# Kernel tuning notes

Measured on AMD Instinct MI355X. Metric: run time of the kernel, lower is better.

## Reference

```python
import jax, jax.numpy as jnp
import numpy as np

NUM_LAYERS = 3
CHANNELS = 8
IN_CHANNELS = 8
MASK_OUT_STRIDE = 4
WEIGHT_NUMS = [(IN_CHANNELS + 2) * CHANNELS, CHANNELS * CHANNELS, CHANNELS]
BIAS_NUMS = [CHANNELS, CHANNELS, 1]
NUM_GEN_PARAMS = sum(WEIGHT_NUMS) + sum(BIAS_NUMS)  # 169
SOI = np.array([64.0, 128.0, 256.0, 512.0, 1024.0], dtype=np.float32)


def compute_locations(h, w, stride):
    # FCOS grid point centers, (H*W, 2) in (x, y) order
    shifts_x = jnp.arange(w, dtype=jnp.float32) * stride + stride // 2
    shifts_y = jnp.arange(h, dtype=jnp.float32) * stride + stride // 2
    ys, xs = jnp.meshgrid(shifts_y, shifts_x, indexing='ij')
    return jnp.stack([xs.reshape(-1), ys.reshape(-1)], axis=1)


def parse_dynamic_params(params):
    # params: (n_inst, 169) -> per-layer weights (n, cout, cin) and biases (n, cout)
    n = params.shape[0]
    split_pts = np.cumsum(WEIGHT_NUMS + BIAS_NUMS)[:-1].tolist()
    splits = jnp.split(params, split_pts, axis=1)
    ws, bs = [], []
    for l in range(NUM_LAYERS):
        cout = CHANNELS if l < NUM_LAYERS - 1 else 1
        ws.append(splits[l].reshape(n, cout, -1))
        bs.append(splits[NUM_LAYERS + l].reshape(n, cout))
    return ws, bs


def aligned_bilinear(x, factor):
    # Faithful port of AdelaiDet aligned_bilinear (replicate pad + align_corners=True bilinear).
    if factor == 1:
        return x
    n, c, h, w = x.shape
    xp = jnp.pad(x, ((0, 0), (0, 0), (0, 1), (0, 1)), mode='edge')  # (n,c,h+1,w+1)
    oh, ow = factor * h + 1, factor * w + 1
    # align_corners=True with oh = factor*h+1 over h+1 samples -> exact coords i/factor
    ys = jnp.arange(oh, dtype=x.dtype) / factor
    xs = jnp.arange(ow, dtype=x.dtype) / factor
    y0 = jnp.floor(ys).astype(jnp.int32)
    y1 = jnp.minimum(y0 + 1, h)
    x0 = jnp.floor(xs).astype(jnp.int32)
    x1 = jnp.minimum(x0 + 1, w)
    wy = (ys - y0.astype(x.dtype))[None, None, :, None]
    wx = (xs - x0.astype(x.dtype))[None, None, None, :]
    rows = xp[:, :, y0, :] * (1 - wy) + xp[:, :, y1, :] * wy
    out = rows[:, :, :, x0] * (1 - wx) + rows[:, :, :, x1] * wx
    pad = factor // 2
    out = jnp.pad(out, ((0, 0), (0, 0), (pad, 0), (pad, 0)), mode='edge')
    return out[:, :, :oh - 1, :ow - 1]  # (n, c, factor*h, factor*w)


def dynamic_head(x, params):
    # x: (n_inst, cin, HW); per-instance 1x1 convs == batched tiny GEMMs
    ws, bs = parse_dynamic_params(params)
    h = x
    for i, (w, b) in enumerate(zip(ws, bs)):
        h = jnp.einsum('noi,nip->nop', w, h) + b[:, :, None]
        if i < NUM_LAYERS - 1:
            h = jax.nn.relu(h)
    return h  # (n_inst, 1, HW)


def setup_inputs() -> dict:
    key = jax.random.key(0)
    k = jax.random.split(key, 6)
    N, H, W, n_inst = 2, 200, 200, 128
    return {
        'mask_feats': jax.random.normal(k[0], (N, IN_CHANNELS, H, W), jnp.float32),
        'mask_head_params': jax.random.normal(k[1], (n_inst, NUM_GEN_PARAMS), jnp.float32) * 0.1,
        'boundary_head_params': jax.random.normal(k[2], (n_inst, NUM_GEN_PARAMS), jnp.float32) * 0.1,
        'instance_locations': jax.random.uniform(k[3], (n_inst, 2), jnp.float32) * 1600.0,
        'im_inds': jax.random.randint(k[4], (n_inst,), 0, N),
        'fpn_levels': jax.random.randint(k[5], (n_inst,), 0, 5),
        'mask_feat_stride': 8,
    }


def reference(mask_feats, mask_head_params, boundary_head_params, instance_locations, im_inds, fpn_levels, mask_feat_stride):
    N, C, H, W = mask_feats.shape
    n_inst = mask_head_params.shape[0]
    locs = compute_locations(H, W, mask_feat_stride)                 # (HW, 2)
    rel = instance_locations[:, None, :] - locs[None, :, :]          # (n, HW, 2)
    rel = jnp.transpose(rel, (0, 2, 1))                              # (n, 2, HW)
    soi = jnp.asarray(SOI)[fpn_levels]                               # (n,)
    rel = (rel / soi[:, None, None]).astype(mask_feats.dtype)
    feats = mask_feats[im_inds].reshape(n_inst, C, H * W)            # per-instance gather
    x = jnp.concatenate([rel, feats], axis=1)                        # (n, C+2, HW)
    factor = mask_feat_stride // MASK_OUT_STRIDE
    m = aligned_bilinear(dynamic_head(x, mask_head_params).reshape(n_inst, 1, H, W), factor)
    bd = aligned_bilinear(dynamic_head(x, boundary_head_params).reshape(n_inst, 1, H, W), factor)
    return jax.nn.sigmoid(m), jax.nn.sigmoid(bd)
```

## Files before the change

kernel.cpp:

```cpp
#include <hip/hip_runtime.h>


#define BLOCK 256
#define Hh 200
#define Ww 200
#define CINCH 8
#define NP 169
#define TH 25
#define MAXR 14
#define OW 400
#define OH 400

typedef float f32x4 __attribute__((ext_vector_type(4)));
typedef float f32x2 __attribute__((ext_vector_type(2)));

__device__ __forceinline__ f32x2 splat2(float v) { f32x2 r; r.x = v; r.y = v; return r; }
__device__ __forceinline__ f32x2 pkfma(f32x2 a, f32x2 b, f32x2 c) {
    return __builtin_elementwise_fma(a, b, c);
}

__global__ __launch_bounds__(BLOCK, 3) void dmh_fused(
    const float* __restrict__ mask_feats,
    const float* __restrict__ mparams,
    const float* __restrict__ bparams,
    const float* __restrict__ ilocs,
    const int*   __restrict__ im_inds,
    const int*   __restrict__ fpn_levels,
    const int*   __restrict__ stride_p,
    float* __restrict__ out,
    int n_inst)
{
    __shared__ __align__(16) float s_par[2 * 192];
    __shared__ __align__(16) float s_m[2][MAXR][Ww];

    const int tid  = threadIdx.x;
    const int tile = blockIdx.x;
    const int inst = blockIdx.y;

    for (int j = tid; j < 2 * NP; j += BLOCK) {
        const int head = (j < NP) ? 0 : 1;
        const int k = j - head * NP;
        const float v = head ? bparams[inst * NP + k] : mparams[inst * NP + k];
        int dst;
        if      (k < 80)  dst = (k / 10) * 12 + (k % 10);
        else if (k < 144) dst = 96 + (k - 80);
        else if (k < 152) dst = 160 + (k - 144);
        else if (k < 160) dst = 168 + (k - 152);
        else if (k < 168) dst = 176 + (k - 160);
        else              dst = 184;
        s_par[head * 192 + dst] = v;
    }

    const int   s    = stride_p[0];
    const int   half = s >> 1;
    const int   im   = im_inds[inst];
    const int   lvl  = fpn_levels[inst];
    const float inv_soi = 1.0f / (float)(64 << lvl);
    const float ixl = ilocs[inst * 2 + 0];
    const float iyl = ilocs[inst * 2 + 1];

    const int i0 = tile * TH;
    const int r_begin = ((i0 > 0) ? (i0 - 1) : 0) >> 1;
    int r_end = ((i0 + TH - 2) >> 1) + 1;
    if (r_end > Hh - 1) r_end = Hh - 1;
    const int nrows = r_end - r_begin + 1;

    __syncthreads();

    const int npx = nrows * Ww;
    const float* fbase = mask_feats + (size_t)im * CINCH * Hh * Ww;

    for (int g = tid * 4; g < npx; g += BLOCK * 4) {
        asm volatile("" ::: "memory");

        const int lr = g / Ww;
        const int c  = g - lr * Ww;
        const int r  = r_begin + lr;

        f32x2 xa[10], xb[10];
        {
            const float ry   = (iyl - (float)(r * s + half)) * inv_soi;
            const float step = -(float)s * inv_soi;
            const float cx0  = (ixl - (float)(c * s + half)) * inv_soi;
            xa[0].x = cx0;            xa[0].y = cx0 + step;
            xb[0].x = cx0 + 2*step;   xb[0].y = cx0 + 3*step;
            xa[1] = splat2(ry);       xb[1] = xa[1];
            const float* fp = fbase + r * Ww + c;
            #pragma unroll
            for (int ch = 0; ch < 8; ch++) {
                const f32x4 f = *(const f32x4*)(fp + ch * (Hh * Ww));
                xa[2 + ch].x = f.x; xa[2 + ch].y = f.y;
                xb[2 + ch].x = f.z; xb[2 + ch].y = f.w;
            }
        }

        #pragma unroll 1
        for (int head = 0; head < 2; head++) {
            const float* P = s_par + head * 192;
            const f32x2 zero = splat2(0.0f);

            f32x2 h1a[8], h1b[8];
            #pragma unroll
            for (int o = 0; o < 8; o++) {
                const f32x4 wa = *(const f32x4*)(P + o * 12);
                const f32x4 wb = *(const f32x4*)(P + o * 12 + 4);
                const float w8 = P[o * 12 + 8];
                const float w9 = P[o * 12 + 9];
                f32x2 aa = splat2(P[168 + o]);
                f32x2 ab = aa;
                aa = pkfma(splat2(wa.x), xa[0], aa); ab = pkfma(splat2(wa.x), xb[0], ab);
                aa = pkfma(splat2(wa.y), xa[1], aa); ab = pkfma(splat2(wa.y), xb[1], ab);
                aa = pkfma(splat2(wa.z), xa[2], aa); ab = pkfma(splat2(wa.z), xb[2], ab);
                aa = pkfma(splat2(wa.w), xa[3], aa); ab = pkfma(splat2(wa.w), xb[3], ab);
                aa = pkfma(splat2(wb.x), xa[4], aa); ab = pkfma(splat2(wb.x), xb[4], ab);
                aa = pkfma(splat2(wb.y), xa[5], aa); ab = pkfma(splat2(wb.y), xb[5], ab);
                aa = pkfma(splat2(wb.z), xa[6], aa); ab = pkfma(splat2(wb.z), xb[6], ab);
                aa = pkfma(splat2(wb.w), xa[7], aa); ab = pkfma(splat2(wb.w), xb[7], ab);
                aa = pkfma(splat2(w8),   xa[8], aa); ab = pkfma(splat2(w8),   xb[8], ab);
                aa = pkfma(splat2(w9),   xa[9], aa); ab = pkfma(splat2(w9),   xb[9], ab);
                h1a[o] = __builtin_elementwise_max(aa, zero);
                h1b[o] = __builtin_elementwise_max(ab, zero);
            }

            f32x2 h2a[8], h2b[8];
            #pragma unroll
            for (int o = 0; o < 8; o++) {
                const f32x4 wa = *(const f32x4*)(P + 96 + o * 8);
                const f32x4 wb = *(const f32x4*)(P + 96 + o * 8 + 4);
                f32x2 aa = splat2(P[176 + o]);
                f32x2 ab = aa;
                aa = pkfma(splat2(wa.x), h1a[0], aa); ab = pkfma(splat2(wa.x), h1b[0], ab);
                aa = pkfma(splat2(wa.y), h1a[1], aa); ab = pkfma(splat2(wa.y), h1b[1], ab);
                aa = pkfma(splat2(wa.z), h1a[2], aa); ab = pkfma(splat2(wa.z), h1b[2], ab);
                aa = pkfma(splat2(wa.w), h1a[3], aa); ab = pkfma(splat2(wa.w), h1b[3], ab);
                aa = pkfma(splat2(wb.x), h1a[4], aa); ab = pkfma(splat2(wb.x), h1b[4], ab);
                aa = pkfma(splat2(wb.y), h1a[5], aa); ab = pkfma(splat2(wb.y), h1b[5], ab);
                aa = pkfma(splat2(wb.z), h1a[6], aa); ab = pkfma(splat2(wb.z), h1b[6], ab);
                aa = pkfma(splat2(wb.w), h1a[7], aa); ab = pkfma(splat2(wb.w), h1b[7], ab);
                h2a[o] = __builtin_elementwise_max(aa, zero);
                h2b[o] = __builtin_elementwise_max(ab, zero);
            }

            const f32x4 wa = *(const f32x4*)(P + 160);
            const f32x4 wb = *(const f32x4*)(P + 164);
            f32x2 aa = splat2(P[184]);
            f32x2 ab = aa;
            aa = pkfma(splat2(wa.x), h2a[0], aa); ab = pkfma(splat2(wa.x), h2b[0], ab);
            aa = pkfma(splat2(wa.y), h2a[1], aa); ab = pkfma(splat2(wa.y), h2b[1], ab);
            aa = pkfma(splat2(wa.z), h2a[2], aa); ab = pkfma(splat2(wa.z), h2b[2], ab);
            aa = pkfma(splat2(wa.w), h2a[3], aa); ab = pkfma(splat2(wa.w), h2b[3], ab);
            aa = pkfma(splat2(wb.x), h2a[4], aa); ab = pkfma(splat2(wb.x), h2b[4], ab);
            aa = pkfma(splat2(wb.y), h2a[5], aa); ab = pkfma(splat2(wb.y), h2b[5], ab);
            aa = pkfma(splat2(wb.z), h2a[6], aa); ab = pkfma(splat2(wb.z), h2b[6], ab);
            aa = pkfma(splat2(wb.w), h2a[7], aa); ab = pkfma(splat2(wb.w), h2b[7], ab);

            f32x4 res;
            res.x = aa.x; res.y = aa.y; res.z = ab.x; res.w = ab.y;
            *(f32x4*)(&s_m[head][lr][c]) = res;
        }
    }

    __syncthreads();

    float* out0 = out + (size_t)inst * (OH * OW) + (size_t)i0 * OW;
    float* out1 = out0 + (size_t)n_inst * (OH * OW);

    const int NU = OW / 8;
    const int ntask = TH * NU;
    for (int t = tid; t < ntask; t += BLOCK) {
        const int row = t / NU;
        const int u   = t - row * NU;
        const int i   = i0 + row;
        const int ip  = (i > 0) ? (i - 1) : 0;
        const int y0  = ip >> 1;
        const float wy = (ip & 1) ? 0.5f : 0.0f;
        const int lr0 = y0 - r_begin;
        const int r1c = (y0 + 1 <= Hh - 1) ? (y0 + 1) : (Hh - 1);
        const int lr1 = r1c - r_begin;

        #pragma unroll
        for (int head = 0; head < 2; head++) {
            const f32x4 A0 = *(const f32x4*)(&s_m[head][lr0][4 * u]);
            const f32x4 A1 = *(const f32x4*)(&s_m[head][lr1][4 * u]);
            float p0 = 0.0f, p1 = 0.0f;
            if (u > 0) {
                p0 = s_m[head][lr0][4 * u - 1];
                p1 = s_m[head][lr1][4 * u - 1];
            }
            f32x4 B;
            B.x = A0.x + (A1.x - A0.x) * wy;
            B.y = A0.y + (A1.y - A0.y) * wy;
            B.z = A0.z + (A1.z - A0.z) * wy;
            B.w = A0.w + (A1.w - A0.w) * wy;
            const float PB = p0 + (p1 - p0) * wy;

            float o[8];
            o[0] = (u > 0) ? 0.5f * (PB + B.x) : B.x;
            o[1] = B.x;
            o[2] = 0.5f * (B.x + B.y);
            o[3] = B.y;
            o[4] = 0.5f * (B.y + B.z);
            o[5] = B.z;
            o[6] = 0.5f * (B.z + B.w);
            o[7] = B.w;

            f32x4 lo, hi;
            #pragma unroll
            for (int k = 0; k < 4; k++) lo[k] = 1.0f / (1.0f + __expf(-o[k]));
            #pragma unroll
            for (int k = 0; k < 4; k++) hi[k] = 1.0f / (1.0f + __expf(-o[4 + k]));

            float* dst = (head ? out1 : out0) + row * OW + 8 * u;
            __builtin_nontemporal_store(lo, (f32x4*)dst);
            __builtin_nontemporal_store(hi, (f32x4*)(dst + 4));
        }
    }
}

extern "C" void kernel_launch(void* const* d_in, const int* in_sizes, int n_in,
                              void* d_out, int out_size, void* d_ws, size_t ws_size,
                              hipStream_t stream) {
    const float* mask_feats = (const float*)d_in[0];
    const float* mparams    = (const float*)d_in[1];
    const float* bparams    = (const float*)d_in[2];
    const float* ilocs      = (const float*)d_in[3];
    const int*   im_inds    = (const int*)d_in[4];
    const int*   fpn_levels = (const int*)d_in[5];
    const int*   stride_p   = (const int*)d_in[6];
    float* out = (float*)d_out;

    const int n_inst = in_sizes[1] / NP;
    dim3 grid(OH / TH, n_inst);
    dim3 block(BLOCK);
    hipLaunchKernelGGL(dmh_fused, grid, block, 0, stream,
                       mask_feats, mparams, bparams, ilocs,
                       im_inds, fpn_levels, stride_p, out, n_inst);
}
```

Baseline: 71.95 us.

## Process two pixel quads per thread with hoisted loads and padded param layout

Replaces the strided per-quad loop in the MLP stage with a fixed schedule: each thread loads two 4-pixel groups up front and runs both through each head together, then a masked third group covers the remainder. The parameter layout in shared memory is re-padded to 16-float rows so layer-1 weights and bias load as three aligned vec4 reads, and the launch-bounds occupancy hint is dropped. The aim is more memory-level parallelism and ILP from issuing all feature loads early. The cost is higher register pressure, which may lower occupancy, and the unrolling assumes at most 768 quads per tile (14 rows × 50 = 700).

```diff
diff --git a/kernel.cpp b/kernel.cpp
--- a/kernel.cpp
+++ b/kernel.cpp
@@ -4,12 +4,12 @@
 #define BLOCK 256
 #define Hh 200
 #define Ww 200
-#define CINCH 8
 #define NP 169
 #define TH 25
 #define MAXR 14
 #define OW 400
 #define OH 400
+#define PSTR 224
 
 typedef float f32x4 __attribute__((ext_vector_type(4)));
 typedef float f32x2 __attribute__((ext_vector_type(2)));
@@ -19,7 +19,143 @@
     return __builtin_elementwise_fma(a, b, c);
 }
 
-__global__ __launch_bounds__(BLOCK, 3) void dmh_fused(
+__device__ __forceinline__ void load_x(
+    int c, int r_begin, const float* __restrict__ fbase,
+    float ixl, float iyl, float inv_soi, int s, int half,
+    f32x2 (&x)[10][2])
+{
+    const int lr = c / (Ww / 4);
+    const int c4 = (c - lr * (Ww / 4)) * 4;
+    const int r  = r_begin + lr;
+    const float ry   = (iyl - (float)(r * s + half)) * inv_soi;
+    const float step = -(float)s * inv_soi;
+    const float cx0  = (ixl - (float)(c4 * s + half)) * inv_soi;
+    x[0][0].x = cx0;            x[0][0].y = cx0 + step;
+    x[0][1].x = cx0 + 2*step;   x[0][1].y = cx0 + 3*step;
+    x[1][0] = splat2(ry);       x[1][1] = x[1][0];
+    const float* fp = fbase + r * Ww + c4;
+    #pragma unroll
+    for (int ch = 0; ch < 8; ch++) {
+        const f32x4 f = *(const f32x4*)(fp + ch * (Hh * Ww));
+        x[2 + ch][0].x = f.x; x[2 + ch][0].y = f.y;
+        x[2 + ch][1].x = f.z; x[2 + ch][1].y = f.w;
+    }
+}
+
+template<bool TWO>
+__device__ __forceinline__ void mlp_head(
+    const float* __restrict__ P,
+    const f32x2 (&xA)[10][2], const f32x2 (&xB)[10][2],
+    f32x2 (&oA)[2], f32x2 (&oB)[2])
+{
+    const f32x2 zero = splat2(0.0f);
+
+    f32x2 h1A[8][2], h1B[8][2];
+    #pragma unroll
+    for (int o = 0; o < 8; o++) {
+        const f32x4 wa = *(const f32x4*)(P + o * 16);
+        const f32x4 wb = *(const f32x4*)(P + o * 16 + 4);
+        const f32x4 wc = *(const f32x4*)(P + o * 16 + 8);
+        #pragma unroll
+        for (int p = 0; p < 2; p++) {
+            f32x2 a = splat2(wc.z);
+            a = pkfma(splat2(wa.x), xA[0][p], a);
+            a = pkfma(splat2(wa.y), xA[1][p], a);
+            a = pkfma(splat2(wa.z), xA[2][p], a);
+            a = pkfma(splat2(wa.w), xA[3][p], a);
+            a = pkfma(splat2(wb.x), xA[4][p], a);
+            a = pkfma(splat2(wb.y), xA[5][p], a);
+            a = pkfma(splat2(wb.z), xA[6][p], a);
+            a = pkfma(splat2(wb.w), xA[7][p], a);
+            a = pkfma(splat2(wc.x), xA[8][p], a);
+            a = pkfma(splat2(wc.y), xA[9][p], a);
+            h1A[o][p] = __builtin_elementwise_max(a, zero);
+            if (TWO) {
+                f32x2 b = splat2(wc.z);
+                b = pkfma(splat2(wa.x), xB[0][p], b);
+                b = pkfma(splat2(wa.y), xB[1][p], b);
+                b = pkfma(splat2(wa.z), xB[2][p], b);
+                b = pkfma(splat2(wa.w), xB[3][p], b);
+                b = pkfma(splat2(wb.x), xB[4][p], b);
+                b = pkfma(splat2(wb.y), xB[5][p], b);
+                b = pkfma(splat2(wb.z), xB[6][p], b);
+                b = pkfma(splat2(wb.w), xB[7][p], b);
+                b = pkfma(splat2(wc.x), xB[8][p], b);
+                b = pkfma(splat2(wc.y), xB[9][p], b);
+                h1B[o][p] = __builtin_elementwise_max(b, zero);
+            }
+        }
+    }
+
+    const f32x4 blo = *(const f32x4*)(P + 192);
+    const f32x4 bhi = *(const f32x4*)(P + 196);
+    const float b1v[8] = {blo.x, blo.y, blo.z, blo.w, bhi.x, bhi.y, bhi.z, bhi.w};
+
+    f32x2 h2A[8][2], h2B[8][2];
+    #pragma unroll
+    for (int o = 0; o < 8; o++) {
+        const f32x4 wa = *(const f32x4*)(P + 128 + o * 8);
+        const f32x4 wb = *(const f32x4*)(P + 128 + o * 8 + 4);
+        #pragma unroll
+        for (int p = 0; p < 2; p++) {
+            f32x2 a = splat2(b1v[o]);
+            a = pkfma(splat2(wa.x), h1A[0][p], a);
+            a = pkfma(splat2(wa.y), h1A[1][p], a);
+            a = pkfma(splat2(wa.z), h1A[2][p], a);
+            a = pkfma(splat2(wa.w), h1A[3][p], a);
+            a = pkfma(splat2(wb.x), h1A[4][p], a);
+            a = pkfma(splat2(wb.y), h1A[5][p], a);
+            a = pkfma(splat2(wb.z), h1A[6][p], a);
+            a = pkfma(splat2(wb.w), h1A[7][p], a);
+            h2A[o][p] = __builtin_elementwise_max(a, zero);
+            if (TWO) {
+                f32x2 b = splat2(b1v[o]);
+                b = pkfma(splat2(wa.x), h1B[0][p], b);
+                b = pkfma(splat2(wa.y), h1B[1][p], b);
+                b = pkfma(splat2(wa.z), h1B[2][p], b);
+                b = pkfma(splat2(wa.w), h1B[3][p], b);
+                b = pkfma(splat2(wb.x), h1B[4][p], b);
+                b = pkfma(splat2(wb.y), h1B[5][p], b);
+                b = pkfma(splat2(wb.z), h1B[6][p], b);
+                b = pkfma(splat2(wb.w), h1B[7][p], b);
+                h2B[o][p] = __builtin_elementwise_max(b, zero);
+            }
+        }
+    }
+
+    {
+        const f32x4 wa = *(const f32x4*)(P + 200);
+        const f32x4 wb = *(const f32x4*)(P + 204);
+        const float b2 = P[208];
+        #pragma unroll
+        for (int p = 0; p < 2; p++) {
+            f32x2 a = splat2(b2);
+            a = pkfma(splat2(wa.x), h2A[0][p], a);
+            a = pkfma(splat2(wa.y), h2A[1][p], a);
+            a = pkfma(splat2(wa.z), h2A[2][p], a);
+            a = pkfma(splat2(wa.w), h2A[3][p], a);
+            a = pkfma(splat2(wb.x), h2A[4][p], a);
+            a = pkfma(splat2(wb.y), h2A[5][p], a);
+            a = pkfma(splat2(wb.z), h2A[6][p], a);
+            a = pkfma(splat2(wb.w), h2A[7][p], a);
+            oA[p] = a;
+            if (TWO) {
+                f32x2 b = splat2(b2);
+                b = pkfma(splat2(wa.x), h2B[0][p], b);
+                b = pkfma(splat2(wa.y), h2B[1][p], b);
+                b = pkfma(splat2(wa.z), h2B[2][p], b);
+                b = pkfma(splat2(wa.w), h2B[3][p], b);
+                b = pkfma(splat2(wb.x), h2B[4][p], b);
+                b = pkfma(splat2(wb.y), h2B[5][p], b);
+                b = pkfma(splat2(wb.z), h2B[6][p], b);
+                b = pkfma(splat2(wb.w), h2B[7][p], b);
+                oB[p] = b;
+            }
+        }
+    }
+}
+
+__global__ __launch_bounds__(BLOCK) void dmh_fused(
     const float* __restrict__ mask_feats,
     const float* __restrict__ mparams,
     const float* __restrict__ bparams,
@@ -30,7 +166,7 @@
     float* __restrict__ out,
     int n_inst)
 {
-    __shared__ __align__(16) float s_par[2 * 192];
+    __shared__ __align__(16) float s_par[2 * PSTR];
     __shared__ __align__(16) float s_m[2][MAXR][Ww];
 
     const int tid  = threadIdx.x;
@@ -42,13 +178,13 @@
         const int k = j - head * NP;
         const float v = head ? bparams[inst * NP + k] : mparams[inst * NP + k];
         int dst;
-        if      (k < 80)  dst = (k / 10) * 12 + (k % 10);
-        else if (k < 144) dst = 96 + (k - 80);
-        else if (k < 152) dst = 160 + (k - 144);
-        else if (k < 160) dst = 168 + (k - 152);
-        else if (k < 168) dst = 176 + (k - 160);
-        else              dst = 184;
-        s_par[head * 192 + dst] = v;
+        if      (k < 80)  dst = (k / 10) * 16 + (k % 10);
+        else if (k < 144) dst = 128 + (k - 80);
+        else if (k < 152) dst = 200 + (k - 144);
+        else if (k < 160) dst = (k - 152) * 16 + 10;
+        else if (k < 168) dst = 192 + (k - 160);
+        else              dst = 208;
+        s_par[head * PSTR + dst] = v;
     }
 
     const int   s    = stride_p[0];
@@ -67,96 +203,48 @@
 
     __syncthreads();
 
-    const int npx = nrows * Ww;
-    const float* fbase = mask_feats + (size_t)im * CINCH * Hh * Ww;
-
-    for (int g = tid * 4; g < npx; g += BLOCK * 4) {
+    const float* fbase = mask_feats + (size_t)im * 8 * Hh * Ww;
+    const int ntask = (nrows * Ww) >> 2;
+
+    {
         asm volatile("" ::: "memory");
-
-        const int lr = g / Ww;
-        const int c  = g - lr * Ww;
-        const int r  = r_begin + lr;
-
-        f32x2 xa[10], xb[10];
-        {
-            const float ry   = (iyl - (float)(r * s + half)) * inv_soi;
-            const float step = -(float)s * inv_soi;
-            const float cx0  = (ixl - (float)(c * s + half)) * inv_soi;
-            xa[0].x = cx0;            xa[0].y = cx0 + step;
-            xb[0].x = cx0 + 2*step;   xb[0].y = cx0 + 3*step;
-            xa[1] = splat2(ry);       xb[1] = xa[1];
-            const float* fp = fbase + r * Ww + c;
-            #pragma unroll
-            for (int ch = 0; ch < 8; ch++) {
-                const f32x4 f = *(const f32x4*)(fp + ch * (Hh * Ww));
-                xa[2 + ch].x = f.x; xa[2 + ch].y = f.y;
-                xb[2 + ch].x = f.z; xb[2 + ch].y = f.w;
-            }
-        }
-
+        f32x2 xA[10][2], xB[10][2];
+        load_x(tid,       r_begin, fbase, ixl, iyl, inv_soi, s, half, xA);
+        load_x(tid + 256, r_begin, fbase, ixl, iyl, inv_soi, s, half, xB);
         #pragma unroll 1
         for (int head = 0; head < 2; head++) {
-            const float* P = s_par + head * 192;
-            const f32x2 zero = splat2(0.0f);
-
-            f32x2 h1a[8], h1b[8];
-            #pragma unroll
-            for (int o = 0; o < 8; o++) {
-                const f32x4 wa = *(const f32x4*)(P + o * 12);
-                const f32x4 wb = *(const f32x4*)(P + o * 12 + 4);
-                const float w8 = P[o * 12 + 8];
-                const float w9 = P[o * 12 + 9];
-                f32x2 aa = splat2(P[168 + o]);
-                f32x2 ab = aa;
-                aa = pkfma(splat2(wa.x), xa[0], aa); ab = pkfma(splat2(wa.x), xb[0], ab);
-                aa = pkfma(splat2(wa.y), xa[1], aa); ab = pkfma(splat2(wa.y), xb[1], ab);
-                aa = pkfma(splat2(wa.z), xa[2], aa); ab = pkfma(splat2(wa.z), xb[2], ab);
-                aa = pkfma(splat2(wa.w), xa[3], aa); ab = pkfma(splat2(wa.w), xb[3], ab);
-                aa = pkfma(splat2(wb.x), xa[4], aa); ab = pkfma(splat2(wb.x), xb[4], ab);
-                aa = pkfma(splat2(wb.y), xa[5], aa); ab = pkfma(splat2(wb.y), xb[5], ab);
-                aa = pkfma(splat2(wb.z), xa[6], aa); ab = pkfma(splat2(wb.z), xb[6], ab);
-                aa = pkfma(splat2(wb.w), xa[7], aa); ab = pkfma(splat2(wb.w), xb[7], ab);
-                aa = pkfma(splat2(w8),   xa[8], aa); ab = pkfma(splat2(w8),   xb[8], ab);
-                aa = pkfma(splat2(w9),   xa[9], aa); ab = pkfma(splat2(w9),   xb[9], ab);
-                h1a[o] = __builtin_elementwise_max(aa, zero);
-                h1b[o] = __builtin_elementwise_max(ab, zero);
-            }
-
-            f32x2 h2a[8], h2b[8];
-            #pragma unroll
-            for (int o = 0; o < 8; o++) {
-                const f32x4 wa = *(const f32x4*)(P + 96 + o * 8);
-                const f32x4 wb = *(const f32x4*)(P + 96 + o * 8 + 4);
-                f32x2 aa = splat2(P[176 + o]);
-                f32x2 ab = aa;
-                aa = pkfma(splat2(wa.x), h1a[0], aa); ab = pkfma(splat2(wa.x), h1b[0], ab);
-                aa = pkfma(splat2(wa.y), h1a[1], aa); ab = pkfma(splat2(wa.y), h1b[1], ab);
-                aa = pkfma(splat2(wa.z), h1a[2], aa); ab = pkfma(splat2(wa.z), h1b[2], ab);
-                aa = pkfma(splat2(wa.w), h1a[3], aa); ab = pkfma(splat2(wa.w), h1b[3], ab);
-                aa = pkfma(splat2(wb.x), h1a[4], aa); ab = pkfma(splat2(wb.x), h1b[4], ab);
-                aa = pkfma(splat2(wb.y), h1a[5], aa); ab = pkfma(splat2(wb.y), h1b[5], ab);
-                aa = pkfma(splat2(wb.z), h1a[6], aa); ab = pkfma(splat2(wb.z), h1b[6], ab);
-                aa = pkfma(splat2(wb.w), h1a[7], aa); ab = pkfma(splat2(wb.w), h1b[7], ab);
-                h2a[o] = __builtin_elementwise_max(aa, zero);
-                h2b[o] = __builtin_elementwise_max(ab, zero);
-            }
-
-            const f32x4 wa = *(const f32x4*)(P + 160);
-            const f32x4 wb = *(const f32x4*)(P + 164);
-            f32x2 aa = splat2(P[184]);
-            f32x2 ab = aa;
-            aa = pkfma(splat2(wa.x), h2a[0], aa); ab = pkfma(splat2(wa.x), h2b[0], ab);
-            aa = pkfma(splat2(wa.y), h2a[1], aa); ab = pkfma(splat2(wa.y), h2b[1], ab);
-            aa = pkfma(splat2(wa.z), h2a[2], aa); ab = pkfma(splat2(wa.z), h2b[2], ab);
-            aa = pkfma(splat2(wa.w), h2a[3], aa); ab = pkfma(splat2(wa.w), h2b[3], ab);
-            aa = pkfma(splat2(wb.x), h2a[4], aa); ab = pkfma(splat2(wb.x), h2b[4], ab);
-            aa = pkfma(splat2(wb.y), h2a[5], aa); ab = pkfma(splat2(wb.y), h2b[5], ab);
-            aa = pkfma(splat2(wb.z), h2a[6], aa); ab = pkfma(splat2(wb.z), h2b[6], ab);
-            aa = pkfma(splat2(wb.w), h2a[7], aa); ab = pkfma(splat2(wb.w), h2b[7], ab);
-
-            f32x4 res;
-            res.x = aa.x; res.y = aa.y; res.z = ab.x; res.w = ab.y;
-            *(f32x4*)(&s_m[head][lr][c]) = res;
+            f32x2 oA[2], oB[2];
+            mlp_head<true>(s_par + head * PSTR, xA, xB, oA, oB);
+            {
+                const int lr = tid / (Ww / 4);
+                const int c4 = (tid - lr * (Ww / 4)) * 4;
+                f32x4 r; r.x = oA[0].x; r.y = oA[0].y; r.z = oA[1].x; r.w = oA[1].y;
+                *(f32x4*)(&s_m[head][lr][c4]) = r;
+            }
+            {
+                const int c2 = tid + 256;
+                const int lr = c2 / (Ww / 4);
+                const int c4 = (c2 - lr * (Ww / 4)) * 4;
+                f32x4 r; r.x = oB[0].x; r.y = oB[0].y; r.z = oB[1].x; r.w = oB[1].y;
+                *(f32x4*)(&s_m[head][lr][c4]) = r;
+            }
+        }
+    }
+    {
+        const int c = tid + 512;
+        if (c < ntask) {
+            asm volatile("" ::: "memory");
+            f32x2 xA[10][2];
+            load_x(c, r_begin, fbase, ixl, iyl, inv_soi, s, half, xA);
+            #pragma unroll 1
+            for (int head = 0; head < 2; head++) {
+                f32x2 oA[2], oB[2];
+                mlp_head<false>(s_par + head * PSTR, xA, xA, oA, oB);
+                const int lr = c / (Ww / 4);
+                const int c4 = (c - lr * (Ww / 4)) * 4;
+                f32x4 r; r.x = oA[0].x; r.y = oA[0].y; r.z = oA[1].x; r.w = oA[1].y;
+                *(f32x4*)(&s_m[head][lr][c4]) = r;
+            }
         }
     }
 
@@ -166,8 +254,8 @@
     float* out1 = out0 + (size_t)n_inst * (OH * OW);
 
     const int NU = OW / 8;
-    const int ntask = TH * NU;
-    for (int t = tid; t < ntask; t += BLOCK) {
+    const int ntaskb = TH * NU;
+    for (int t = tid; t < ntaskb; t += BLOCK) {
         const int row = t / NU;
         const int u   = t - row * NU;
         const int i   = i0 + row;
```

Result: slower. 95.04 us (+32.1%).

## Prepack duplicated weight pairs in a pre-kernel and read them via scalar loads

Applied to the files above, without the earlier changes.

Adds a small repack kernel that writes each instance's dynamic-head parameters to workspace in a padded layout, with every weight and bias duplicated into a float2 pair. The main kernel then reads these weights directly from global memory (uniform per block, so likely scalar loads) instead of staging them in LDS, and uses the pairs as packed-FMA operands without splat moves. This removes the per-block LDS parameter load and one barrier, and avoids splat/broadcast instructions. The cost is an extra kernel launch, more scalar-register pressure or memory latency on weight loads inside the pixel loop, and a dependency on the workspace buffer.

```diff
diff --git a/kernel.cpp b/kernel.cpp
--- a/kernel.cpp
+++ b/kernel.cpp
@@ -4,12 +4,12 @@
 #define BLOCK 256
 #define Hh 200
 #define Ww 200
-#define CINCH 8
 #define NP 169
 #define TH 25
 #define MAXR 14
 #define OW 400
 #define OH 400
+#define HSTR 384
 
 typedef float f32x4 __attribute__((ext_vector_type(4)));
 typedef float f32x2 __attribute__((ext_vector_type(2)));
@@ -19,10 +19,34 @@
     return __builtin_elementwise_fma(a, b, c);
 }
 
+__global__ __launch_bounds__(BLOCK) void repack_params(
+    const float* __restrict__ mparams,
+    const float* __restrict__ bparams,
+    float* __restrict__ wsf)
+{
+    const int inst = blockIdx.x;
+    const int t = threadIdx.x;
+    #pragma unroll
+    for (int head = 0; head < 2; head++) {
+        if (t < NP) {
+            const float v = (head ? bparams : mparams)[inst * NP + t];
+            const int k = t;
+            int dst;
+            if      (k < 80)  { const int o = k / 10;       dst = o * 24 + 2 * (k - 10 * o); }
+            else if (k < 144) { const int kk = k - 80;      dst = 192 + (kk >> 3) * 20 + 2 * (kk & 7); }
+            else if (k < 152) { dst = 352 + 2 * (k - 144); }
+            else if (k < 160) { dst = (k - 152) * 24 + 20; }
+            else if (k < 168) { dst = 192 + (k - 160) * 20 + 16; }
+            else              { dst = 352 + 16; }
+            float* p = wsf + (size_t)(inst * 2 + head) * HSTR + dst;
+            p[0] = v; p[1] = v;
+        }
+    }
+}
+
 __global__ __launch_bounds__(BLOCK, 3) void dmh_fused(
     const float* __restrict__ mask_feats,
-    const float* __restrict__ mparams,
-    const float* __restrict__ bparams,
+    const float* __restrict__ wsf,
     const float* __restrict__ ilocs,
     const int*   __restrict__ im_inds,
     const int*   __restrict__ fpn_levels,
@@ -30,26 +54,11 @@
     float* __restrict__ out,
     int n_inst)
 {
-    __shared__ __align__(16) float s_par[2 * 192];
     __shared__ __align__(16) float s_m[2][MAXR][Ww];
 
     const int tid  = threadIdx.x;
     const int tile = blockIdx.x;
     const int inst = blockIdx.y;
-
-    for (int j = tid; j < 2 * NP; j += BLOCK) {
-        const int head = (j < NP) ? 0 : 1;
-        const int k = j - head * NP;
-        const float v = head ? bparams[inst * NP + k] : mparams[inst * NP + k];
-        int dst;
-        if      (k < 80)  dst = (k / 10) * 12 + (k % 10);
-        else if (k < 144) dst = 96 + (k - 80);
-        else if (k < 152) dst = 160 + (k - 144);
-        else if (k < 160) dst = 168 + (k - 152);
-        else if (k < 168) dst = 176 + (k - 160);
-        else              dst = 184;
-        s_par[head * 192 + dst] = v;
-    }
 
     const int   s    = stride_p[0];
     const int   half = s >> 1;
@@ -65,10 +74,8 @@
     if (r_end > Hh - 1) r_end = Hh - 1;
     const int nrows = r_end - r_begin + 1;
 
-    __syncthreads();
-
+    const float* fbase = mask_feats + (size_t)im * 8 * Hh * Ww;
     const int npx = nrows * Ww;
-    const float* fbase = mask_feats + (size_t)im * CINCH * Hh * Ww;
 
     for (int g = tid * 4; g < npx; g += BLOCK * 4) {
         asm volatile("" ::: "memory");
@@ -77,86 +84,90 @@
         const int c  = g - lr * Ww;
         const int r  = r_begin + lr;
 
-        f32x2 xa[10], xb[10];
+        f32x2 x[10][2];
         {
             const float ry   = (iyl - (float)(r * s + half)) * inv_soi;
             const float step = -(float)s * inv_soi;
             const float cx0  = (ixl - (float)(c * s + half)) * inv_soi;
-            xa[0].x = cx0;            xa[0].y = cx0 + step;
-            xb[0].x = cx0 + 2*step;   xb[0].y = cx0 + 3*step;
-            xa[1] = splat2(ry);       xb[1] = xa[1];
+            x[0][0].x = cx0;            x[0][0].y = cx0 + step;
+            x[0][1].x = cx0 + 2*step;   x[0][1].y = cx0 + 3*step;
+            x[1][0] = splat2(ry);       x[1][1] = x[1][0];
             const float* fp = fbase + r * Ww + c;
             #pragma unroll
             for (int ch = 0; ch < 8; ch++) {
                 const f32x4 f = *(const f32x4*)(fp + ch * (Hh * Ww));
-                xa[2 + ch].x = f.x; xa[2 + ch].y = f.y;
-                xb[2 + ch].x = f.z; xb[2 + ch].y = f.w;
+                x[2 + ch][0].x = f.x; x[2 + ch][0].y = f.y;
+                x[2 + ch][1].x = f.z; x[2 + ch][1].y = f.w;
             }
         }
 
         #pragma unroll 1
         for (int head = 0; head < 2; head++) {
-            const float* P = s_par + head * 192;
+            const float* P = wsf + (size_t)(inst * 2 + head) * HSTR;
             const f32x2 zero = splat2(0.0f);
 
-            f32x2 h1a[8], h1b[8];
+            f32x2 h1[8][2];
             #pragma unroll
             for (int o = 0; o < 8; o++) {
-                const f32x4 wa = *(const f32x4*)(P + o * 12);
-                const f32x4 wb = *(const f32x4*)(P + o * 12 + 4);
-                const float w8 = P[o * 12 + 8];
-                const float w9 = P[o * 12 + 9];
-                f32x2 aa = splat2(P[168 + o]);
-                f32x2 ab = aa;
-                aa = pkfma(splat2(wa.x), xa[0], aa); ab = pkfma(splat2(wa.x), xb[0], ab);
-                aa = pkfma(splat2(wa.y), xa[1], aa); ab = pkfma(splat2(wa.y), xb[1], ab);
-                aa = pkfma(splat2(wa.z), xa[2], aa); ab = pkfma(splat2(wa.z), xb[2], ab);
-                aa = pkfma(splat2(wa.w), xa[3], aa); ab = pkfma(splat2(wa.w), xb[3], ab);
-                aa = pkfma(splat2(wb.x), xa[4], aa); ab = pkfma(splat2(wb.x), xb[4], ab);
-                aa = pkfma(splat2(wb.y), xa[5], aa); ab = pkfma(splat2(wb.y), xb[5], ab);
-                aa = pkfma(splat2(wb.z), xa[6], aa); ab = pkfma(splat2(wb.z), xb[6], ab);
-                aa = pkfma(splat2(wb.w), xa[7], aa); ab = pkfma(splat2(wb.w), xb[7], ab);
-                aa = pkfma(splat2(w8),   xa[8], aa); ab = pkfma(splat2(w8),   xb[8], ab);
-                aa = pkfma(splat2(w9),   xa[9], aa); ab = pkfma(splat2(w9),   xb[9], ab);
-                h1a[o] = __builtin_elementwise_max(aa, zero);
-                h1b[o] = __builtin_elementwise_max(ab, zero);
-            }
-
-            f32x2 h2a[8], h2b[8];
+                const f32x2* __restrict__ R = (const f32x2*)(P + o * 24);
+                const f32x2 b = R[10];
+                #pragma unroll
+                for (int p = 0; p < 2; p++) {
+                    f32x2 a = b;
+                    a = pkfma(R[0], x[0][p], a);
+                    a = pkfma(R[1], x[1][p], a);
+                    a = pkfma(R[2], x[2][p], a);
+                    a = pkfma(R[3], x[3][p], a);
+                    a = pkfma(R[4], x[4][p], a);
+                    a = pkfma(R[5], x[5][p], a);
+                    a = pkfma(R[6], x[6][p], a);
+                    a = pkfma(R[7], x[7][p], a);
+                    a = pkfma(R[8], x[8][p], a);
+                    a = pkfma(R[9], x[9][p], a);
+                    h1[o][p] = __builtin_elementwise_max(a, zero);
+                }
+            }
+
+            f32x2 h2[8][2];
             #pragma unroll
             for (int o = 0; o < 8; o++) {
-                const f32x4 wa = *(const f32x4*)(P + 96 + o * 8);
-                const f32x4 wb = *(const f32x4*)(P + 96 + o * 8 + 4);
-                f32x2 aa = splat2(P[176 + o]);
-                f32x2 ab = aa;
-                aa = pkfma(splat2(wa.x), h1a[0], aa); ab = pkfma(splat2(wa.x), h1b[0], ab);
-                aa = pkfma(splat2(wa.y), h1a[1], aa); ab = pkfma(splat2(wa.y), h1b[1], ab);
-                aa = pkfma(splat2(wa.z), h1a[2], aa); ab = pkfma(splat2(wa.z), h1b[2], ab);
-                aa = pkfma(splat2(wa.w), h1a[3], aa); ab = pkfma(splat2(wa.w), h1b[3], ab);
-                aa = pkfma(splat2(wb.x), h1a[4], aa); ab = pkfma(splat2(wb.x), h1b[4], ab);
-                aa = pkfma(splat2(wb.y), h1a[5], aa); ab = pkfma(splat2(wb.y), h1b[5], ab);
-                aa = pkfma(splat2(wb.z), h1a[6], aa); ab = pkfma(splat2(wb.z), h1b[6], ab);
-                aa = pkfma(splat2(wb.w), h1a[7], aa); ab = pkfma(splat2(wb.w), h1b[7], ab);
-                h2a[o] = __builtin_elementwise_max(aa, zero);
-                h2b[o] = __builtin_elementwise_max(ab, zero);
-            }
-
-            const f32x4 wa = *(const f32x4*)(P + 160);
-            const f32x4 wb = *(const f32x4*)(P + 164);
-            f32x2 aa = splat2(P[184]);
-            f32x2 ab = aa;
-            aa = pkfma(splat2(wa.x), h2a[0], aa); ab = pkfma(splat2(wa.x), h2b[0], ab);
-            aa = pkfma(splat2(wa.y), h2a[1], aa); ab = pkfma(splat2(wa.y), h2b[1], ab);
-            aa = pkfma(splat2(wa.z), h2a[2], aa); ab = pkfma(splat2(wa.z), h2b[2], ab);
-            aa = pkfma(splat2(wa.w), h2a[3], aa); ab = pkfma(splat2(wa.w), h2b[3], ab);
-            aa = pkfma(splat2(wb.x), h2a[4], aa); ab = pkfma(splat2(wb.x), h2b[4], ab);
-            aa = pkfma(splat2(wb.y), h2a[5], aa); ab = pkfma(splat2(wb.y), h2b[5], ab);
-            aa = pkfma(splat2(wb.z), h2a[6], aa); ab = pkfma(splat2(wb.z), h2b[6], ab);
-            aa = pkfma(splat2(wb.w), h2a[7], aa); ab = pkfma(splat2(wb.w), h2b[7], ab);
-
-            f32x4 res;
-            res.x = aa.x; res.y = aa.y; res.z = ab.x; res.w = ab.y;
-            *(f32x4*)(&s_m[head][lr][c]) = res;
+                const f32x2* __restrict__ R = (const f32x2*)(P + 192 + o * 20);
+                const f32x2 b = R[8];
+                #pragma unroll
+                for (int p = 0; p < 2; p++) {
+                    f32x2 a = b;
+                    a = pkfma(R[0], h1[0][p], a);
+                    a = pkfma(R[1], h1[1][p], a);
+                    a = pkfma(R[2], h1[2][p], a);
+                    a = pkfma(R[3], h1[3][p], a);
+                    a = pkfma(R[4], h1[4][p], a);
+                    a = pkfma(R[5], h1[5][p], a);
+                    a = pkfma(R[6], h1[6][p], a);
+                    a = pkfma(R[7], h1[7][p], a);
+                    h2[o][p] = __builtin_elementwise_max(a, zero);
+                }
+            }
+
+            {
+                const f32x2* __restrict__ R = (const f32x2*)(P + 352);
+                const f32x2 b = R[8];
+                f32x4 res;
+                #pragma unroll
+                for (int p = 0; p < 2; p++) {
+                    f32x2 a = b;
+                    a = pkfma(R[0], h2[0][p], a);
+                    a = pkfma(R[1], h2[1][p], a);
+                    a = pkfma(R[2], h2[2][p], a);
+                    a = pkfma(R[3], h2[3][p], a);
+                    a = pkfma(R[4], h2[4][p], a);
+                    a = pkfma(R[5], h2[5][p], a);
+                    a = pkfma(R[6], h2[6][p], a);
+                    a = pkfma(R[7], h2[7][p], a);
+                    res[2 * p]     = a.x;
+                    res[2 * p + 1] = a.y;
+                }
+                *(f32x4*)(&s_m[head][lr][c]) = res;
+            }
         }
     }
 
@@ -166,8 +177,8 @@
     float* out1 = out0 + (size_t)n_inst * (OH * OW);
 
     const int NU = OW / 8;
-    const int ntask = TH * NU;
-    for (int t = tid; t < ntask; t += BLOCK) {
+    const int ntaskb = TH * NU;
+    for (int t = tid; t < ntaskb; t += BLOCK) {
         const int row = t / NU;
         const int u   = t - row * NU;
         const int i   = i0 + row;
@@ -228,11 +239,15 @@
     const int*   fpn_levels = (const int*)d_in[5];
     const int*   stride_p   = (const int*)d_in[6];
     float* out = (float*)d_out;
+    float* wsf = (float*)d_ws;
 
     const int n_inst = in_sizes[1] / NP;
+
+    hipLaunchKernelGGL(repack_params, dim3(n_inst), dim3(BLOCK), 0, stream,
+                       mparams, bparams, wsf);
+
     dim3 grid(OH / TH, n_inst);
-    dim3 block(BLOCK);
-    hipLaunchKernelGGL(dmh_fused, grid, block, 0, stream,
-                       mask_feats, mparams, bparams, ilocs,
+    hipLaunchKernelGGL(dmh_fused, grid, dim3(BLOCK), 0, stream,
+                       mask_feats, wsf, ilocs,
                        im_inds, fpn_levels, stride_p, out, n_inst);
 }
```

After: 78.67 us. 1.09x slower.
